# Optimization experiments

Hardware: AMD Instinct MI355X
Metric: run time of the kernel (lower is better)

Reference implementation:

```python
import jax, jax.numpy as jnp
import numpy as np

B, LP, NC, D, E = 8, 1000, 64, 128, 320  # batch, protein len, compound atoms, hid dim, esm dim


def _linear_params(key, din, dout):
    k1, k2 = jax.random.split(key)
    lim = 1.0 / np.sqrt(din)
    W = jax.random.uniform(k1, (din, dout), minval=-lim, maxval=lim, dtype=jnp.float32)
    b = jax.random.uniform(k2, (dout,), minval=-lim, maxval=lim, dtype=jnp.float32)
    return W, b


def setup_inputs() -> dict:
    key = jax.random.key(0)
    ks = jax.random.split(key, 14)
    inp = {
        "protein_embedding": jax.random.normal(ks[0], (B, LP, E), dtype=jnp.float32),
        "protein_feat_x": jax.random.normal(ks[1], (B, LP, D), dtype=jnp.float32),
        "compound_feats": jax.random.normal(ks[2], (B, NC, D), dtype=jnp.float32),
    }
    layers = [("emb", E, D), ("wq", D, D), ("wk", D, D), ("wv", D, D), ("wo", D, D),
              ("jp", D, D), ("jc", D, D),
              ("c1", D, 1024), ("c2", 1024, 1024), ("c3", 1024, 256), ("c4", 256, 1)]
    for i, (name, din, dout) in enumerate(layers):
        W, b = _linear_params(ks[3 + i], din, dout)
        inp[name + "_w"] = W
        inp[name + "_b"] = b
    return inp


def reference(protein_embedding, protein_feat_x, compound_feats,
              emb_w, emb_b, wq_w, wq_b, wk_w, wk_b, wv_w, wv_b, wo_w, wo_b,
              jp_w, jp_b, jc_w, jc_b,
              c1_w, c1_b, c2_w, c2_b, c3_w, c3_b, c4_w, c4_b):
    # protein sequence embedding -> hid dim
    pe = protein_embedding @ emb_w + emb_b                      # [B, LP, D]
    # single-head cross attention: query = seq embedding, key/value = graph feats
    Q = pe @ wq_w + wq_b
    K = protein_feat_x @ wk_w + wk_b
    V = protein_feat_x @ wv_w + wv_b
    scale = jnp.sqrt(jnp.asarray(D, pe.dtype))                  # n_heads=1 -> head_dim=D
    attn = jax.nn.softmax(jnp.einsum('bqd,bkd->bqk', Q, K) / scale, axis=-1)
    protein_feats = jnp.einsum('bqk,bkd->bqd', attn, V) @ wo_w + wo_b  # [B, LP, D]

    # sigmoid bilinear joint attention over (protein residue, compound atom) pairs
    P = jax.nn.relu(protein_feats) @ jp_w + jp_b                # [B, LP, D]
    C = jax.nn.relu(compound_feats) @ jc_w + jc_b               # [B, NC, D]
    A = jax.nn.sigmoid(jnp.einsum('bid,bkd->bik', P, C))        # [B, LP, NC]
    A = A / jnp.sum(A, axis=(1, 2), keepdims=True)

    # tanh outer product (the costly 4D bikj intermediate) then weighted reduction
    cp = jnp.tanh(protein_feats[:, :, None, :] * compound_feats[:, None, :, :])  # [B, LP, NC, D]
    cp_embedding = jnp.einsum('bikd,bik->bd', cp, A)            # [B, D]

    # classifier MLP (dropout is eval-mode identity)
    h = jax.nn.relu(cp_embedding @ c1_w + c1_b)
    h = jax.nn.relu(h @ c2_w + c2_b)
    h = jax.nn.relu(h @ c3_w + c3_b)
    return h @ c4_w + c4_b                                      # [B, 1]
```

## Files before the change

### kernel.cpp

```cpp
#include <hip/hip_runtime.h>
#include <hip/hip_bf16.h>
#include <math.h>

#define LP 1000
#define NCMP 64
#define NSPLIT 4

typedef _Float16 f16;
typedef f16   v8h __attribute__((ext_vector_type(8)));
typedef float v4f __attribute__((ext_vector_type(4)));

__device__ __forceinline__ float rcp_fast(float x) { return __builtin_amdgcn_rcpf(x); }
__device__ __forceinline__ void fsplit(float x, f16& h, f16& l) {
    h = (f16)x; l = (f16)(x - (float)h);
}

struct H4 { f16 a, b, c, d; };

__device__ __forceinline__ void gemm_core(float (*Ws)[128], float (*Xt)[36],
                                          const float* X, const float* W, const float* bias,
                                          float* Y, int K, int rowbase, bool relu_in)
{
    const int t  = threadIdx.x;
    const int r0 = (t >> 5) * 4;
    const int c0 = (t & 31) * 4;
    const int xr = t >> 3, xk = (t & 7) << 2;
    const int xrow = rowbase + xr;
    float4 xv = *(const float4*)(X + (long)xrow * K + xk);
    float4 wv[4];
    #pragma unroll
    for (int u = 0; u < 4; ++u) {
        int s = t + u * 256, r = s >> 5, cb = (s & 31) << 2;
        wv[u] = *(const float4*)(W + (long)r * 128 + cb);
    }
    float acc[4][4] = {};
    for (int k0 = 0; k0 < K; k0 += 32) {
        float4 xs = xv;
        if (relu_in) { xs.x = fmaxf(xs.x,0.f); xs.y = fmaxf(xs.y,0.f);
                       xs.z = fmaxf(xs.z,0.f); xs.w = fmaxf(xs.w,0.f); }
        Xt[xk+0][xr] = xs.x; Xt[xk+1][xr] = xs.y; Xt[xk+2][xr] = xs.z; Xt[xk+3][xr] = xs.w;
        #pragma unroll
        for (int u = 0; u < 4; ++u) {
            int s = t + u * 256, r = s >> 5, cb = (s & 31) << 2;
            *(float4*)&Ws[r][cb] = wv[u];
        }
        __syncthreads();
        if (k0 + 32 < K) {
            xv = *(const float4*)(X + (long)xrow * K + k0 + 32 + xk);
            #pragma unroll
            for (int u = 0; u < 4; ++u) {
                int s = t + u * 256, r = s >> 5, cb = (s & 31) << 2;
                wv[u] = *(const float4*)(W + (long)(k0 + 32 + r) * 128 + cb);
            }
        }
        #pragma unroll
        for (int kk = 0; kk < 32; ++kk) {
            float4 w4 = *(const float4*)&Ws[kk][c0];
            float4 x4 = *(const float4*)&Xt[kk][r0];
            acc[0][0] = fmaf(x4.x, w4.x, acc[0][0]); acc[0][1] = fmaf(x4.x, w4.y, acc[0][1]);
            acc[0][2] = fmaf(x4.x, w4.z, acc[0][2]); acc[0][3] = fmaf(x4.x, w4.w, acc[0][3]);
            acc[1][0] = fmaf(x4.y, w4.x, acc[1][0]); acc[1][1] = fmaf(x4.y, w4.y, acc[1][1]);
            acc[1][2] = fmaf(x4.y, w4.z, acc[1][2]); acc[1][3] = fmaf(x4.y, w4.w, acc[1][3]);
            acc[2][0] = fmaf(x4.z, w4.x, acc[2][0]); acc[2][1] = fmaf(x4.z, w4.y, acc[2][1]);
            acc[2][2] = fmaf(x4.z, w4.z, acc[2][2]); acc[2][3] = fmaf(x4.z, w4.w, acc[2][3]);
            acc[3][0] = fmaf(x4.w, w4.x, acc[3][0]); acc[3][1] = fmaf(x4.w, w4.y, acc[3][1]);
            acc[3][2] = fmaf(x4.w, w4.z, acc[3][2]); acc[3][3] = fmaf(x4.w, w4.w, acc[3][3]);
        }
        __syncthreads();
    }
    float4 bv = bias ? *(const float4*)(bias + c0) : make_float4(0.f,0.f,0.f,0.f);
    #pragma unroll
    for (int i = 0; i < 4; ++i) {
        int row = rowbase + r0 + i;
        float4 o;
        o.x = acc[i][0] + bv.x; o.y = acc[i][1] + bv.y;
        o.z = acc[i][2] + bv.z; o.w = acc[i][3] + bv.w;
        *(float4*)(Y + (long)row * 128 + c0) = o;
    }
}

__global__ __launch_bounds__(256) void pre0_k(const float* __restrict__ emb_w, const float* __restrict__ emb_b,
                                              const float* __restrict__ wq_w, const float* __restrict__ wq_b,
                                              const float* __restrict__ wv_w, const float* __restrict__ wv_b,
                                              const float* __restrict__ wo_w, const float* __restrict__ wo_b,
                                              float* __restrict__ Wp, float* __restrict__ bp,
                                              float* __restrict__ Wvo, float* __restrict__ bvo,
                                              float* __restrict__ zbase)
{
    __shared__ __align__(16) float Ws[32][128];
    __shared__ __align__(16) float Xt[32][36];
    const int bid = blockIdx.x;
    if (bid < 10) { gemm_core(Ws, Xt, emb_w, wq_w, nullptr, Wp, 128, bid * 32, false); return; }
    if (bid >= 11 && bid < 15) { gemm_core(Ws, Xt, wv_w, wo_w, nullptr, Wvo, 128, (bid - 11) * 32, false); return; }
    int t = threadIdx.x;
    if (bid == 10 && t >= 128) {
        for (int i = t - 128; i < 1032; i += 128) zbase[i] = 0.f;
        return;
    }
    if (t < 128) {
        const float* vb = (bid == 10) ? emb_b : wv_b;
        const float* Wm = (bid == 10) ? wq_w  : wo_w;
        const float* ab = (bid == 10) ? wq_b  : wo_b;
        float a0 = 0.f, a1 = 0.f, a2 = 0.f, a3 = 0.f;
        for (int k = 0; k < 128; k += 4) {
            a0 = fmaf(vb[k+0], Wm[(k+0)*128 + t], a0);
            a1 = fmaf(vb[k+1], Wm[(k+1)*128 + t], a1);
            a2 = fmaf(vb[k+2], Wm[(k+2)*128 + t], a2);
            a3 = fmaf(vb[k+3], Wm[(k+3)*128 + t], a3);
        }
        float* dst = (bid == 10) ? bp : bvo;
        dst[t] = (a0 + a1) + (a2 + a3) + ab[t];
    }
}

__global__ __launch_bounds__(256) void split_k(
    const float* __restrict__ PE, const float* __restrict__ PFX,
    const float* __restrict__ Wp, const float* __restrict__ wk_w,
    f16* __restrict__ PEhi, f16* __restrict__ PElo,
    f16* __restrict__ PXhi, f16* __restrict__ PXlo,
    f16* __restrict__ Vthi, f16* __restrict__ Vtlo,
    f16* __restrict__ WpThi, f16* __restrict__ WpTlo,
    f16* __restrict__ WkThi, f16* __restrict__ WkTlo)
{
    const int bid = blockIdx.x, t = threadIdx.x;
    if (bid < 250) {
        #pragma unroll
        for (int u = 0; u < 10; ++u) {
            int f = t + u * 256, r = f / 80, c = (f - r * 80) * 4;
            int grow = bid * 32 + r;
            int bb = grow / 1000, rr = grow - bb * 1000;
            float4 v = *(const float4*)(PE + (long)grow * 320 + c);
            H4 h, l;
            fsplit(v.x, h.a, l.a); fsplit(v.y, h.b, l.b);
            fsplit(v.z, h.c, l.c); fsplit(v.w, h.d, l.d);
            long o = ((long)bb * 1024 + rr) * 320 + c;
            *(H4*)(PEhi + o) = h; *(H4*)(PElo + o) = l;
        }
        return;
    }
    if (bid < 500) {
        const int rb = (bid - 250) * 32;
        #pragma unroll
        for (int u = 0; u < 4; ++u) {
            int f = t + u * 256, r = f >> 5, c = (f & 31) * 4;
            int grow = rb + r;
            int bb = grow / 1000, rr = grow - bb * 1000;
            float4 v = *(const float4*)(PFX + (long)grow * 128 + c);
            H4 h, l;
            fsplit(v.x, h.a, l.a); fsplit(v.y, h.b, l.b);
            fsplit(v.z, h.c, l.c); fsplit(v.w, h.d, l.d);
            long o = ((long)bb * 1024 + rr) * 128 + c;
            *(H4*)(PXhi + o) = h; *(H4*)(PXlo + o) = l;
        }
        const int d = t >> 1, half = t & 1;
        #pragma unroll 4
        for (int i = 0; i < 16; ++i) {
            int row = rb + half * 16 + i;
            int bb = row / 1000, rr = row - bb * 1000;
            float v = PFX[(long)row * 128 + d];
            f16 h, l; fsplit(v, h, l);
            long o = ((long)bb * 128 + d) * 1024 + rr;
            Vthi[o] = h; Vtlo[o] = l;
        }
        return;
    }
    #pragma unroll
    for (int u = 0; u < 8; ++u) {
        int idx = (bid - 500) * 2048 + u * 256 + t;
        if (idx < 40960) {
            int k = idx >> 7, n = idx & 127;
            f16 h, l; fsplit(Wp[idx], h, l);
            WpThi[(long)n * 320 + k] = h; WpTlo[(long)n * 320 + k] = l;
        } else {
            int j = idx - 40960;
            int k = j >> 7, n = j & 127;
            f16 h, l; fsplit(wk_w[j], h, l);
            WkThi[(long)n * 128 + k] = h; WkTlo[(long)n * 128 + k] = l;
        }
    }
}

__global__ __launch_bounds__(256) void qkv2_k(
    const f16* __restrict__ PEhi, const f16* __restrict__ PElo,
    const f16* __restrict__ PXhi, const f16* __restrict__ PXlo,
    const f16* __restrict__ WpThi, const f16* __restrict__ WpTlo,
    const f16* __restrict__ WkThi, const f16* __restrict__ WkTlo,
    const float* __restrict__ bp, const float* __restrict__ wk_b,
    const float* __restrict__ CF, const float* __restrict__ jc_w, const float* __restrict__ jc_b,
    f16* __restrict__ Qhi, f16* __restrict__ Qlo,
    f16* __restrict__ Khi, f16* __restrict__ Klo,
    float* __restrict__ Cj)
{
    __shared__ __align__(16) float Ws[32][128];
    __shared__ __align__(16) float Xt[32][36];
    const int bid = blockIdx.x;
    if (bid >= 256) { gemm_core(Ws, Xt, CF, jc_w, jc_b, Cj, 128, (bid - 256) * 32, true); return; }
    const bool isQ = bid < 128;
    const int b = (bid & 127) >> 4, tile = bid & 15;
    const int KD  = isQ ? 320 : 128;
    const int NCH = isQ ? 10 : 4;
    const f16* Ahi = isQ ? PEhi : PXhi;
    const f16* Alo = isQ ? PElo : PXlo;
    const f16* Bhi = isQ ? WpThi : WkThi;
    const f16* Blo = isQ ? WpTlo : WkTlo;
    const float* bias = isQ ? bp : wk_b;
    f16* Yhi = isQ ? Qhi : Khi;
    f16* Ylo = isQ ? Qlo : Klo;

    const int t = threadIdx.x;
    const int wv = t >> 6, lane = t & 63, quad = lane >> 4, l4 = lane & 15;
    int arow = tile * 64 + wv * 16 + l4; if (arow >= LP) arow = LP - 1;
    const f16* ah_p = Ahi + ((long)b * 1024 + arow) * KD;
    const f16* al_p = Alo + ((long)b * 1024 + arow) * KD;

    v4f acc[8];
    #pragma unroll
    for (int dt = 0; dt < 8; ++dt) acc[dt] = (v4f){0.f, 0.f, 0.f, 0.f};

    for (int kt = 0; kt < NCH; ++kt) {
        const int ko = kt * 32 + quad * 8;
        v8h ah = *(const v8h*)(ah_p + ko);
        v8h al = *(const v8h*)(al_p + ko);
        #pragma unroll
        for (int dt = 0; dt < 8; ++dt) {
            const long bo = (long)(dt * 16 + l4) * KD + ko;
            v8h bh = *(const v8h*)(Bhi + bo);
            v8h bl = *(const v8h*)(Blo + bo);
            acc[dt] = __builtin_amdgcn_mfma_f32_16x16x32_f16(ah, bh, acc[dt], 0, 0, 0);
            acc[dt] = __builtin_amdgcn_mfma_f32_16x16x32_f16(ah, bl, acc[dt], 0, 0, 0);
            acc[dt] = __builtin_amdgcn_mfma_f32_16x16x32_f16(al, bh, acc[dt], 0, 0, 0);
        }
    }
    #pragma unroll
    for (int dt = 0; dt < 8; ++dt) {
        const int col = dt * 16 + l4;
        const float bv = bias[col];
        #pragma unroll
        for (int r = 0; r < 4; ++r) {
            int row = tile * 64 + wv * 16 + quad * 4 + r;
            long o = ((long)b * 1024 + row) * 128 + col;
            f16 h, l; fsplit(acc[dt][r] + bv, h, l);
            Yhi[o] = h; Ylo[o] = l;
        }
    }
}

__global__ __launch_bounds__(256) void flash7_k(const f16* __restrict__ Qhi, const f16* __restrict__ Qlo,
                                                const f16* __restrict__ Khi, const f16* __restrict__ Klo,
                                                const f16* __restrict__ Vthi, const f16* __restrict__ Vtlo,
                                                float* __restrict__ Opart,
                                                float* __restrict__ mpart, float* __restrict__ lpart)
{
    __shared__ __align__(16) f16 KVhi[9216];
    __shared__ __align__(16) f16 KVlo[9216];
    __shared__ __align__(16) f16 Pshi[4][16 * 72];
    __shared__ __align__(16) f16 Pslo[4][16 * 72];
    const int t    = threadIdx.x;
    const int wv   = t >> 6;
    const int lane = t & 63;
    const int quad = lane >> 4;
    const int l4   = lane & 15;
    const int qt = blockIdx.x, sp = blockIdx.y, b = blockIdx.z;
    const int q0 = qt * 64;
    const float SCALE = 0.08838834764831845f;
    const float L2E   = 1.4426950408889634f;

    int qrow = q0 + wv * 16 + l4; if (qrow >= LP) qrow = LP - 1;
    const long qbase = ((long)b * 1024 + qrow) * 128;
    v8h qh[4], ql[4];
    #pragma unroll
    for (int kt4 = 0; kt4 < 4; ++kt4) {
        qh[kt4] = *(const v8h*)(Qhi + qbase + kt4 * 32 + quad * 8);
        ql[kt4] = *(const v8h*)(Qlo + qbase + kt4 * 32 + quad * 8);
    }
    float m_i[4] = { -3.0e38f, -3.0e38f, -3.0e38f, -3.0e38f };
    float l_i[4] = { 0.f, 0.f, 0.f, 0.f };
    v4f  O[8];
    #pragma unroll
    for (int dt = 0; dt < 8; ++dt) O[dt] = (v4f){0.f, 0.f, 0.f, 0.f};

    for (int kt = sp * 4; kt < sp * 4 + 4; ++kt) {
        const int key0 = kt * 64;
        __syncthreads();
        #pragma unroll
        for (int u = 0; u < 4; ++u) {
            int ch = t + u * 256;
            int r = ch >> 4, co = (ch & 15) * 8;
            long ga = ((long)b * 1024 + key0 + r) * 128 + co;
            *(v8h*)(KVhi + r * 136 + co) = *(const v8h*)(Khi + ga);
            *(v8h*)(KVlo + r * 136 + co) = *(const v8h*)(Klo + ga);
        }
        __syncthreads();
        v8h vh[4], vl[4];
        #pragma unroll
        for (int u = 0; u < 4; ++u) {
            int ch = t + u * 256;
            int d = ch >> 3, co = (ch & 7) * 8;
            long ga = ((long)b * 128 + d) * 1024 + key0 + co;
            vh[u] = *(const v8h*)(Vthi + ga);
            vl[u] = *(const v8h*)(Vtlo + ga);
        }
        v4f S[4];
        #pragma unroll
        for (int nt = 0; nt < 4; ++nt) S[nt] = (v4f){0.f, 0.f, 0.f, 0.f};
        #pragma unroll
        for (int nt = 0; nt < 4; ++nt) {
            const int rb = (nt * 16 + l4) * 136;
            #pragma unroll
            for (int kt4 = 0; kt4 < 4; ++kt4) {
                v8h bh = *(const v8h*)(KVhi + rb + kt4 * 32 + quad * 8);
                v8h bl = *(const v8h*)(KVlo + rb + kt4 * 32 + quad * 8);
                S[nt] = __builtin_amdgcn_mfma_f32_16x16x32_f16(qh[kt4], bh, S[nt], 0, 0, 0);
                S[nt] = __builtin_amdgcn_mfma_f32_16x16x32_f16(qh[kt4], bl, S[nt], 0, 0, 0);
                S[nt] = __builtin_amdgcn_mfma_f32_16x16x32_f16(ql[kt4], bh, S[nt], 0, 0, 0);
            }
        }
        #pragma unroll
        for (int nt = 0; nt < 4; ++nt) {
            bool valid = (key0 + nt * 16 + l4) < LP;
            #pragma unroll
            for (int r = 0; r < 4; ++r)
                S[nt][r] = valid ? S[nt][r] * SCALE : -3.0e38f;
        }
        float alpha[4];
        #pragma unroll
        for (int r = 0; r < 4; ++r) {
            float tm = fmaxf(fmaxf(S[0][r], S[1][r]), fmaxf(S[2][r], S[3][r]));
            tm = fmaxf(tm, __shfl_xor(tm, 1));
            tm = fmaxf(tm, __shfl_xor(tm, 2));
            tm = fmaxf(tm, __shfl_xor(tm, 4));
            tm = fmaxf(tm, __shfl_xor(tm, 8));
            float mnew = fmaxf(m_i[r], tm);
            alpha[r] = exp2f((m_i[r] - mnew) * L2E);
            float ps = 0.f;
            #pragma unroll
            for (int nt = 0; nt < 4; ++nt) {
                float p = exp2f((S[nt][r] - mnew) * L2E);
                S[nt][r] = p;
                ps += p;
            }
            ps += __shfl_xor(ps, 1);
            ps += __shfl_xor(ps, 2);
            ps += __shfl_xor(ps, 4);
            ps += __shfl_xor(ps, 8);
            l_i[r] = l_i[r] * alpha[r] + ps;
            m_i[r] = mnew;
        }
        #pragma unroll
        for (int dt = 0; dt < 8; ++dt) {
            O[dt][0] *= alpha[0]; O[dt][1] *= alpha[1];
            O[dt][2] *= alpha[2]; O[dt][3] *= alpha[3];
        }
        __syncthreads();
        #pragma unroll
        for (int u = 0; u < 4; ++u) {
            int ch = t + u * 256;
            int d = ch >> 3, co = (ch & 7) * 8;
            *(v8h*)(KVhi + d * 72 + co) = vh[u];
            *(v8h*)(KVlo + d * 72 + co) = vl[u];
        }
        #pragma unroll
        for (int nt = 0; nt < 4; ++nt) {
            int col = nt * 16 + l4;
            #pragma unroll
            for (int r = 0; r < 4; ++r) {
                f16 ph, pl; fsplit(S[nt][r], ph, pl);
                Pshi[wv][(quad * 4 + r) * 72 + col] = ph;
                Pslo[wv][(quad * 4 + r) * 72 + col] = pl;
            }
        }
        __syncthreads();
        #pragma unroll
        for (int kc = 0; kc < 2; ++kc) {
            v8h pah = *(const v8h*)(Pshi[wv] + l4 * 72 + kc * 32 + quad * 8);
            v8h pal = *(const v8h*)(Pslo[wv] + l4 * 72 + kc * 32 + quad * 8);
            #pragma unroll
            for (int dt = 0; dt < 8; ++dt) {
                v8h vfh = *(const v8h*)(KVhi + (dt * 16 + l4) * 72 + kc * 32 + quad * 8);
                v8h vfl = *(const v8h*)(KVlo + (dt * 16 + l4) * 72 + kc * 32 + quad * 8);
                O[dt] = __builtin_amdgcn_mfma_f32_16x16x32_f16(pah, vfh, O[dt], 0, 0, 0);
                O[dt] = __builtin_amdgcn_mfma_f32_16x16x32_f16(pah, vfl, O[dt], 0, 0, 0);
                O[dt] = __builtin_amdgcn_mfma_f32_16x16x32_f16(pal, vfh, O[dt], 0, 0, 0);
            }
        }
    }
    #pragma unroll
    for (int r = 0; r < 4; ++r) {
        int row = q0 + wv * 16 + quad * 4 + r;
        if (row < LP) {
            long base = (long)sp * 1024000 + ((long)b * LP + row) * 128;
            #pragma unroll
            for (int dt = 0; dt < 8; ++dt)
                Opart[base + dt * 16 + l4] = O[dt][r];
            if (l4 == 0) {
                mpart[(long)sp * 8000 + b * LP + row] = m_i[r];
                lpart[(long)sp * 8000 + b * LP + row] = l_i[r];
            }
        }
    }
}

__global__ __launch_bounds__(256) void mt1a_k(
    const float* __restrict__ Opart, const float* __restrict__ mp, const float* __restrict__ lp,
    const float* __restrict__ Wvo, const float* __restrict__ bvo, float* __restrict__ PF)
{
    __shared__ __align__(16) float Ws[128][128];
    __shared__ __align__(16) float Xs[16][132];
    const int t  = threadIdx.x;
    const int p0 = blockIdx.x * 16;
    const int b  = blockIdx.y;
    const float L2E = 1.4426950408889634f;

    #pragma unroll
    for (int u = 0; u < 16; ++u) {
        int s = t + u * 256, r = s >> 5, cb = (s & 31) << 2;
        *(float4*)&Ws[r][cb] = *(const float4*)(Wvo + (long)r * 128 + cb);
    }
    {
        const int pr = t >> 4, pc = (t & 15) << 3;
        int grow = p0 + pr; if (grow > LP - 1) grow = LP - 1;
        const long g = (long)b * LP + grow;
        float mm = -3.0e38f;
        #pragma unroll
        for (int s = 0; s < NSPLIT; ++s) mm = fmaxf(mm, mp[g + (long)s * 8000]);
        float wgt[NSPLIT]; float ls = 0.f;
        #pragma unroll
        for (int s = 0; s < NSPLIT; ++s) {
            wgt[s] = exp2f((mp[g + (long)s * 8000] - mm) * L2E);
            ls += wgt[s] * lp[g + (long)s * 8000];
        }
        const float linv = 1.0f / ls;
        float4 a0 = make_float4(0.f,0.f,0.f,0.f), a1 = make_float4(0.f,0.f,0.f,0.f);
        #pragma unroll
        for (int s = 0; s < NSPLIT; ++s) {
            const float* src = Opart + (long)s * 1024000 + g * 128 + pc;
            float4 p = *(const float4*)src;
            float4 q = *(const float4*)(src + 4);
            a0.x = fmaf(wgt[s], p.x, a0.x); a0.y = fmaf(wgt[s], p.y, a0.y);
            a0.z = fmaf(wgt[s], p.z, a0.z); a0.w = fmaf(wgt[s], p.w, a0.w);
            a1.x = fmaf(wgt[s], q.x, a1.x); a1.y = fmaf(wgt[s], q.y, a1.y);
            a1.z = fmaf(wgt[s], q.z, a1.z); a1.w = fmaf(wgt[s], q.w, a1.w);
        }
        *(float4*)&Xs[pr][pc]     = make_float4(a0.x*linv, a0.y*linv, a0.z*linv, a0.w*linv);
        *(float4*)&Xs[pr][pc + 4] = make_float4(a1.x*linv, a1.y*linv, a1.z*linv, a1.w*linv);
    }
    __syncthreads();
    const int r0 = (t >> 5) * 2;
    const int c0 = (t & 31) * 4;
    float acc[2][4] = {};
    #pragma unroll 8
    for (int kk4 = 0; kk4 < 128; kk4 += 4) {
        float4 xa = *(const float4*)&Xs[r0 + 0][kk4];
        float4 xb = *(const float4*)&Xs[r0 + 1][kk4];
        #pragma unroll
        for (int j = 0; j < 4; ++j) {
            float4 w4 = *(const float4*)&Ws[kk4 + j][c0];
            float x0 = (j==0)?xa.x:(j==1)?xa.y:(j==2)?xa.z:xa.w;
            float x1 = (j==0)?xb.x:(j==1)?xb.y:(j==2)?xb.z:xb.w;
            acc[0][0]=fmaf(x0,w4.x,acc[0][0]); acc[0][1]=fmaf(x0,w4.y,acc[0][1]);
            acc[0][2]=fmaf(x0,w4.z,acc[0][2]); acc[0][3]=fmaf(x0,w4.w,acc[0][3]);
            acc[1][0]=fmaf(x1,w4.x,acc[1][0]); acc[1][1]=fmaf(x1,w4.y,acc[1][1]);
            acc[1][2]=fmaf(x1,w4.z,acc[1][2]); acc[1][3]=fmaf(x1,w4.w,acc[1][3]);
        }
    }
    float4 bv = *(const float4*)(bvo + c0);
    #pragma unroll
    for (int i = 0; i < 2; ++i) {
        int orow = p0 + r0 + i;
        if (orow < LP)
            *(float4*)(PF + ((long)b * LP + orow) * 128 + c0) =
                make_float4(acc[i][0]+bv.x, acc[i][1]+bv.y, acc[i][2]+bv.z, acc[i][3]+bv.w);
    }
}

__global__ __launch_bounds__(256) void mt1b_k(
    const float* __restrict__ PF, const float* __restrict__ jp_w, const float* __restrict__ jp_b,
    float* __restrict__ PJ)
{
    __shared__ __align__(16) float Ws[128][128];
    __shared__ __align__(16) float Xs[16][132];
    const int t  = threadIdx.x;
    const int p0 = blockIdx.x * 16;
    const int b  = blockIdx.y;

    #pragma unroll
    for (int u = 0; u < 16; ++u) {
        int s = t + u * 256, r = s >> 5, cb = (s & 31) << 2;
        *(float4*)&Ws[r][cb] = *(const float4*)(jp_w + (long)r * 128 + cb);
    }
    {
        const int pr = t >> 4, pc = (t & 15) << 3;
        int grow = p0 + pr; if (grow > LP - 1) grow = LP - 1;
        const float* src = PF + ((long)b * LP + grow) * 128 + pc;
        float4 p = *(const float4*)src;
        float4 q = *(const float4*)(src + 4);
        *(float4*)&Xs[pr][pc] =
            make_float4(fmaxf(p.x,0.f), fmaxf(p.y,0.f), fmaxf(p.z,0.f), fmaxf(p.w,0.f));
        *(float4*)&Xs[pr][pc + 4] =
            make_float4(fmaxf(q.x,0.f), fmaxf(q.y,0.f), fmaxf(q.z,0.f), fmaxf(q.w,0.f));
    }
    __syncthreads();
    const int r0 = (t >> 5) * 2;
    const int c0 = (t & 31) * 4;
    float acc[2][4] = {};
    #pragma unroll 8
    for (int kk4 = 0; kk4 < 128; kk4 += 4) {
        float4 xa = *(const float4*)&Xs[r0 + 0][kk4];
        float4 xb = *(const float4*)&Xs[r0 + 1][kk4];
        #pragma unroll
        for (int j = 0; j < 4; ++j) {
            float4 w4 = *(const float4*)&Ws[kk4 + j][c0];
            float x0 = (j==0)?xa.x:(j==1)?xa.y:(j==2)?xa.z:xa.w;
            float x1 = (j==0)?xb.x:(j==1)?xb.y:(j==2)?xb.z:xb.w;
            acc[0][0]=fmaf(x0,w4.x,acc[0][0]); acc[0][1]=fmaf(x0,w4.y,acc[0][1]);
            acc[0][2]=fmaf(x0,w4.z,acc[0][2]); acc[0][3]=fmaf(x0,w4.w,acc[0][3]);
            acc[1][0]=fmaf(x1,w4.x,acc[1][0]); acc[1][1]=fmaf(x1,w4.y,acc[1][1]);
            acc[1][2]=fmaf(x1,w4.z,acc[1][2]); acc[1][3]=fmaf(x1,w4.w,acc[1][3]);
        }
    }
    float4 bv = *(const float4*)(jp_b + c0);
    #pragma unroll
    for (int i = 0; i < 2; ++i) {
        int orow = p0 + r0 + i;
        if (orow < LP)
            *(float4*)(PJ + ((long)b * LP + orow) * 128 + c0) =
                make_float4(acc[i][0]+bv.x, acc[i][1]+bv.y, acc[i][2]+bv.z, acc[i][3]+bv.w);
    }
}

template<int IIN>
__device__ __forceinline__ float tanh_chunk(const float (*Cs)[132], const float (*AshT)[20],
                                            const float* areg, int d, int kh)
{
    float accD = 0.f;
    for (int kk = 0; kk < 16; ++kk) {
        const int k = (kh << 4) + kk;
        const float cv = Cs[k][d];
        #pragma unroll
        for (int iq = 0; iq < IIN; iq += 4) {
            float4 a4 = *(const float4*)&AshT[k][iq];
            float e0 = exp2f(areg[iq+0] * cv);
            float e1 = exp2f(areg[iq+1] * cv);
            float e2 = exp2f(areg[iq+2] * cv);
            float e3 = exp2f(areg[iq+3] * cv);
            accD = fmaf(1.f - 2.f * rcp_fast(e0 + 1.f), a4.x, accD);
            accD = fmaf(1.f - 2.f * rcp_fast(e1 + 1.f), a4.y, accD);
            accD = fmaf(1.f - 2.f * rcp_fast(e2 + 1.f), a4.z, accD);
            accD = fmaf(1.f - 2.f * rcp_fast(e3 + 1.f), a4.w, accD);
        }
    }
    return accD;
}

__global__ __launch_bounds__(256) void mt2_k(
    const float* __restrict__ PF, const float* __restrict__ PJ,
    const float* __restrict__ Cj, const float* __restrict__ CF,
    float* __restrict__ Asum, float* __restrict__ cpe)
{
    __shared__ __align__(16) float Pjs[16][132];
    __shared__ __align__(16) float Pfs[16][132];
    __shared__ __align__(16) float Cs[32][132];
    __shared__ __align__(16) float AshT[32][20];
    __shared__ float red[256];
    const int t  = threadIdx.x;
    const int p0 = blockIdx.x * 16;
    const int kc = blockIdx.y;
    const int b  = blockIdx.z;
    const float L2E = 1.4426950408889634f;

    {
        int pr = t >> 4, pc = (t & 15) << 3;
        int gr = p0 + pr; if (gr > LP - 1) gr = LP - 1;
        long gb = ((long)b * LP + gr) * 128 + pc;
        *(float4*)&Pjs[pr][pc]     = *(const float4*)(PJ + gb);
        *(float4*)&Pjs[pr][pc + 4] = *(const float4*)(PJ + gb + 4);
        *(float4*)&Pfs[pr][pc]     = *(const float4*)(PF + gb);
        *(float4*)&Pfs[pr][pc + 4] = *(const float4*)(PF + gb + 4);
    }
    float4 cfv[4];
    #pragma unroll
    for (int u = 0; u < 4; ++u) {
        int s = t + u * 256, r = s >> 5, cb = (s & 31) << 2;
        *(float4*)&Cs[r][cb] = *(const float4*)(Cj + ((long)b * NCMP + kc * 32 + r) * 128 + cb);
        cfv[u] = *(const float4*)(CF + ((long)b * NCMP + kc * 32 + r) * 128 + cb);
    }
    __syncthreads();
    const int tr = t >> 4, tc = t & 15;
    float sacc[2] = {0.f, 0.f};
    #pragma unroll 4
    for (int d4 = 0; d4 < 32; ++d4) {
        float4 p4 = *(const float4*)&Pjs[tr][d4 << 2];
        #pragma unroll
        for (int j = 0; j < 2; ++j) {
            float4 cv = *(const float4*)&Cs[tc + (j << 4)][d4 << 2];
            sacc[j] += p4.x*cv.x + p4.y*cv.y + p4.z*cv.z + p4.w*cv.w;
        }
    }
    float lsum = 0.f;
    const int gi = p0 + tr;
    #pragma unroll
    for (int j = 0; j < 2; ++j) {
        float sg = rcp_fast(1.f + exp2f(-sacc[j] * L2E));
        if (gi < LP) { AshT[tc + (j << 4)][tr] = sg; lsum += sg; }
    }
    #pragma unroll
    for (int off = 1; off < 64; off <<= 1) lsum += __shfl_xor(lsum, off);
    if ((t & 63) == 0) red[t >> 6] = lsum;
    __syncthreads();
    if (t == 0) atomicAdd(Asum + b, (red[0] + red[1]) + (red[2] + red[3]));
    #pragma unroll
    for (int u = 0; u < 4; ++u) {
        int s = t + u * 256, r = s >> 5, cb = (s & 31) << 2;
        *(float4*)&Cs[r][cb] = cfv[u];
    }
    __syncthreads();
    const float TWO_L2E = 2.8853900817779268f;
    const int d = t & 127, kh = t >> 7;
    float areg[16];
    #pragma unroll
    for (int ii = 0; ii < 16; ++ii) areg[ii] = Pfs[ii][d] * TWO_L2E;
    float accD = (p0 + 16 <= LP) ? tanh_chunk<16>(Cs, AshT, areg, d, kh)
                                 : tanh_chunk<8>(Cs, AshT, areg, d, kh);
    red[t] = accD;
    __syncthreads();
    if (t < 128) atomicAdd(cpe + (long)b * 128 + t, red[t] + red[t + 128]);
}

__global__ __launch_bounds__(256) void c12_k(const float* __restrict__ cpe, const float* __restrict__ Asum,
                                             const float* __restrict__ c1_w, const float* __restrict__ c1_b,
                                             const float* __restrict__ c2_w, float* __restrict__ part)
{
    __shared__ float sc[8][128];
    __shared__ float ins[8][8];
    const int t = threadIdx.x, ks = blockIdx.x, k0 = ks * 8;
    #pragma unroll
    for (int u = 0; u < 4; ++u) {
        int idx = t + u * 256;
        sc[idx >> 7][idx & 127] = cpe[idx] * rcp_fast(Asum[idx >> 7]);
    }
    __syncthreads();
    if (t < 64) {
        int b = t >> 3, kk = t & 7;
        int n1 = k0 + kk;
        float a0 = 0.f, a1 = 0.f, a2 = 0.f, a3 = 0.f;
        #pragma unroll 8
        for (int j = 0; j < 128; j += 4) {
            a0 = fmaf(sc[b][j+0], c1_w[(long)(j+0)*1024 + n1], a0);
            a1 = fmaf(sc[b][j+1], c1_w[(long)(j+1)*1024 + n1], a1);
            a2 = fmaf(sc[b][j+2], c1_w[(long)(j+2)*1024 + n1], a2);
            a3 = fmaf(sc[b][j+3], c1_w[(long)(j+3)*1024 + n1], a3);
        }
        ins[b][kk] = fmaxf((a0 + a1) + (a2 + a3) + c1_b[n1], 0.f);
    }
    __syncthreads();
    const int n = (t & 63) * 4 + (t >> 6) * 256;
    float4 acc[8] = {};
    #pragma unroll
    for (int kk = 0; kk < 8; ++kk) {
        float4 w4 = *(const float4*)(c2_w + (long)(k0 + kk) * 1024 + n);
        #pragma unroll
        for (int b = 0; b < 8; ++b) {
            float s = ins[b][kk];
            acc[b].x = fmaf(s, w4.x, acc[b].x); acc[b].y = fmaf(s, w4.y, acc[b].y);
            acc[b].z = fmaf(s, w4.z, acc[b].z); acc[b].w = fmaf(s, w4.w, acc[b].w);
        }
    }
    #pragma unroll
    for (int b = 0; b < 8; ++b)
        *(float4*)(part + ((long)(ks * 8 + b)) * 1024 + n) = acc[b];
}

__global__ __launch_bounds__(256) void c3m_k(const float* __restrict__ part2, const float* __restrict__ c2_b,
                                             const float* __restrict__ c3_w, const float* __restrict__ c3_b,
                                             const float* __restrict__ c4_w, const float* __restrict__ c4_b,
                                             float* __restrict__ out)
{
    __shared__ float Hs[1024];
    __shared__ float red[256];
    const int t = threadIdx.x, b = blockIdx.x;
    float4 acc4 = make_float4(0.f,0.f,0.f,0.f);
    #pragma unroll 4
    for (int ks = 0; ks < 128; ++ks) {
        float4 p = *(const float4*)(part2 + ((long)(ks * 8 + b)) * 1024 + t * 4);
        acc4.x += p.x; acc4.y += p.y; acc4.z += p.z; acc4.w += p.w;
    }
    {
        float4 bb = *(const float4*)(c2_b + t * 4);
        Hs[t*4+0] = fmaxf(acc4.x + bb.x, 0.f);
        Hs[t*4+1] = fmaxf(acc4.y + bb.y, 0.f);
        Hs[t*4+2] = fmaxf(acc4.z + bb.z, 0.f);
        Hs[t*4+3] = fmaxf(acc4.w + bb.w, 0.f);
    }
    __syncthreads();
    float a0 = 0.f, a1 = 0.f, a2 = 0.f, a3 = 0.f;
    #pragma unroll 8
    for (int k = 0; k < 1024; k += 4) {
        a0 = fmaf(Hs[k+0], c3_w[(long)(k+0)*256 + t], a0);
        a1 = fmaf(Hs[k+1], c3_w[(long)(k+1)*256 + t], a1);
        a2 = fmaf(Hs[k+2], c3_w[(long)(k+2)*256 + t], a2);
        a3 = fmaf(Hs[k+3], c3_w[(long)(k+3)*256 + t], a3);
    }
    float h3v = fmaxf((a0 + a1) + (a2 + a3) + c3_b[t], 0.f);
    red[t] = h3v * c4_w[t];
    __syncthreads();
    for (int off = 128; off > 0; off >>= 1) {
        if (t < off) red[t] += red[t + off];
        __syncthreads();
    }
    if (t == 0) out[b] = red[0] + c4_b[0];
}

extern "C" void kernel_launch(void* const* d_in, const int* in_sizes, int n_in,
                              void* d_out, int out_size, void* d_ws, size_t ws_size,
                              hipStream_t stream)
{
    const float* PE   = (const float*)d_in[0];
    const float* PFX  = (const float*)d_in[1];
    const float* CF   = (const float*)d_in[2];
    const float* emb_w = (const float*)d_in[3];  const float* emb_b = (const float*)d_in[4];
    const float* wq_w  = (const float*)d_in[5];  const float* wq_b  = (const float*)d_in[6];
    const float* wk_w  = (const float*)d_in[7];  const float* wk_b  = (const float*)d_in[8];
    const float* wv_w  = (const float*)d_in[9];  const float* wv_b  = (const float*)d_in[10];
    const float* wo_w  = (const float*)d_in[11]; const float* wo_b  = (const float*)d_in[12];
    const float* jp_w  = (const float*)d_in[13]; const float* jp_b  = (const float*)d_in[14];
    const float* jc_w  = (const float*)d_in[15]; const float* jc_b  = (const float*)d_in[16];
    const float* c1_w  = (const float*)d_in[17]; const float* c1_b  = (const float*)d_in[18];
    const float* c2_w  = (const float*)d_in[19]; const float* c2_b  = (const float*)d_in[20];
    const float* c3_w  = (const float*)d_in[21]; const float* c3_b  = (const float*)d_in[22];
    const float* c4_w  = (const float*)d_in[23]; const float* c4_b  = (const float*)d_in[24];

    float* ws     = (float*)d_ws;
    f16*  Qhi   = (f16*)ws;
    f16*  Qlo   = (f16*)(ws + 524288);
    f16*  Khi   = (f16*)(ws + 1048576);
    f16*  Klo   = (f16*)(ws + 1572864);
    f16*  Vthi  = (f16*)(ws + 2097152);
    f16*  Vtlo  = (f16*)(ws + 2621440);
    float* bufC   = ws + 3145728;
    float* Opart  = bufC + 65536;
    float* mpart  = Opart + 4096000;
    float* lpart  = mpart + 32000;
    float* Asum   = lpart + 32000;
    float* cpe    = Asum + 8;
    float* bprime = cpe + 1024;
    float* bufWp  = bprime + 128;
    float* bufWvo = bufWp + 40960;
    float* bufbvo = bufWvo + 16384;
    float* part2  = ws;
    float* PFbuf  = ws + 1048576;
    float* PJbuf  = ws + 2097152;
    f16* PEhi  = (f16*)(ws + 7430144);
    f16* PElo  = (f16*)(ws + 8740864);
    f16* PXhi  = (f16*)(ws + 10051584);
    f16* PXlo  = (f16*)(ws + 10575872);
    f16* WpThi = (f16*)(ws + 11100160);
    f16* WpTlo = (f16*)(ws + 11120640);
    f16* WkThi = (f16*)(ws + 11141120);
    f16* WkTlo = (f16*)(ws + 11149312);

    pre0_k<<<16, 256, 0, stream>>>(emb_w, emb_b, wq_w, wq_b, wv_w, wv_b, wo_w, wo_b,
                                   bufWp, bprime, bufWvo, bufbvo, Asum);
    split_k<<<528, 256, 0, stream>>>(PE, PFX, bufWp, wk_w,
                                     PEhi, PElo, PXhi, PXlo, Vthi, Vtlo,
                                     WpThi, WpTlo, WkThi, WkTlo);
    qkv2_k<<<272, 256, 0, stream>>>(PEhi, PElo, PXhi, PXlo,
                                    WpThi, WpTlo, WkThi, WkTlo,
                                    bprime, wk_b, CF, jc_w, jc_b,
                                    Qhi, Qlo, Khi, Klo, bufC);
    flash7_k<<<dim3(16, NSPLIT, 8), 256, 0, stream>>>(Qhi, Qlo, Khi, Klo, Vthi, Vtlo,
                                                      Opart, mpart, lpart);
    mt1a_k<<<dim3(63, 8), 256, 0, stream>>>(Opart, mpart, lpart, bufWvo, bufbvo, PFbuf);
    mt1b_k<<<dim3(63, 8), 256, 0, stream>>>(PFbuf, jp_w, jp_b, PJbuf);
    mt2_k<<<dim3(63, 2, 8), 256, 0, stream>>>(PFbuf, PJbuf, bufC, CF, Asum, cpe);
    c12_k<<<128, 256, 0, stream>>>(cpe, Asum, c1_w, c1_b, c2_w, part2);
    c3m_k<<<8, 256, 0, stream>>>(part2, c2_b, c3_w, c3_b, c4_w, c4_b, (float*)d_out);
}
```

Before: 282.3 us.

## Fuse fp16 hi/lo split into QKV GEMM and merge mt1a/mt1b kernels

The QKV MFMA kernel now reads the fp32 protein embedding and graph features directly and splits them into fp16 hi/lo pairs in registers. This removes the separate pass that wrote PEhi/PElo/PXhi/PXlo to global memory and read them back. The attention-output projection and the jp projection kernels are also merged into one kernel, which passes the relu'd PF tile through shared memory instead of reloading it from global memory. In exchange the GEMM does redundant conversion work per tile, and one launch is dropped.

```diff
diff --git a/kernel.cpp b/kernel.cpp
--- a/kernel.cpp
+++ b/kernel.cpp
@@ -13,6 +13,15 @@
 __device__ __forceinline__ float rcp_fast(float x) { return __builtin_amdgcn_rcpf(x); }
 __device__ __forceinline__ void fsplit(float x, f16& h, f16& l) {
     h = (f16)x; l = (f16)(x - (float)h);
+}
+__device__ __forceinline__ void fs8(const float4& f0, const float4& f1, v8h& h, v8h& l) {
+    const float x[8] = {f0.x, f0.y, f0.z, f0.w, f1.x, f1.y, f1.z, f1.w};
+    #pragma unroll
+    for (int i = 0; i < 8; ++i) {
+        f16 hh = (f16)x[i];
+        h[i] = hh;
+        l[i] = (f16)(x[i] - (float)hh);
+    }
 }
 
 struct H4 { f16 a, b, c, d; };
@@ -113,45 +122,15 @@
     }
 }
 
-__global__ __launch_bounds__(256) void split_k(
-    const float* __restrict__ PE, const float* __restrict__ PFX,
-    const float* __restrict__ Wp, const float* __restrict__ wk_w,
-    f16* __restrict__ PEhi, f16* __restrict__ PElo,
-    f16* __restrict__ PXhi, f16* __restrict__ PXlo,
+__global__ __launch_bounds__(256) void prep_k(
+    const float* __restrict__ PFX, const float* __restrict__ Wp, const float* __restrict__ wk_w,
     f16* __restrict__ Vthi, f16* __restrict__ Vtlo,
     f16* __restrict__ WpThi, f16* __restrict__ WpTlo,
     f16* __restrict__ WkThi, f16* __restrict__ WkTlo)
 {
     const int bid = blockIdx.x, t = threadIdx.x;
     if (bid < 250) {
-        #pragma unroll
-        for (int u = 0; u < 10; ++u) {
-            int f = t + u * 256, r = f / 80, c = (f - r * 80) * 4;
-            int grow = bid * 32 + r;
-            int bb = grow / 1000, rr = grow - bb * 1000;
-            float4 v = *(const float4*)(PE + (long)grow * 320 + c);
-            H4 h, l;
-            fsplit(v.x, h.a, l.a); fsplit(v.y, h.b, l.b);
-            fsplit(v.z, h.c, l.c); fsplit(v.w, h.d, l.d);
-            long o = ((long)bb * 1024 + rr) * 320 + c;
-            *(H4*)(PEhi + o) = h; *(H4*)(PElo + o) = l;
-        }
-        return;
-    }
-    if (bid < 500) {
-        const int rb = (bid - 250) * 32;
-        #pragma unroll
-        for (int u = 0; u < 4; ++u) {
-            int f = t + u * 256, r = f >> 5, c = (f & 31) * 4;
-            int grow = rb + r;
-            int bb = grow / 1000, rr = grow - bb * 1000;
-            float4 v = *(const float4*)(PFX + (long)grow * 128 + c);
-            H4 h, l;
-            fsplit(v.x, h.a, l.a); fsplit(v.y, h.b, l.b);
-            fsplit(v.z, h.c, l.c); fsplit(v.w, h.d, l.d);
-            long o = ((long)bb * 1024 + rr) * 128 + c;
-            *(H4*)(PXhi + o) = h; *(H4*)(PXlo + o) = l;
-        }
+        const int rb = bid * 32;
         const int d = t >> 1, half = t & 1;
         #pragma unroll 4
         for (int i = 0; i < 16; ++i) {
@@ -166,12 +145,12 @@
     }
     #pragma unroll
     for (int u = 0; u < 8; ++u) {
-        int idx = (bid - 500) * 2048 + u * 256 + t;
+        int idx = (bid - 250) * 2048 + u * 256 + t;
         if (idx < 40960) {
             int k = idx >> 7, n = idx & 127;
             f16 h, l; fsplit(Wp[idx], h, l);
             WpThi[(long)n * 320 + k] = h; WpTlo[(long)n * 320 + k] = l;
-        } else {
+        } else if (idx < 57344) {
             int j = idx - 40960;
             int k = j >> 7, n = j & 127;
             f16 h, l; fsplit(wk_w[j], h, l);
@@ -180,9 +159,8 @@
     }
 }
 
-__global__ __launch_bounds__(256) void qkv2_k(
-    const f16* __restrict__ PEhi, const f16* __restrict__ PElo,
-    const f16* __restrict__ PXhi, const f16* __restrict__ PXlo,
+__global__ __launch_bounds__(256) void qkv3_k(
+    const float* __restrict__ PE, const float* __restrict__ PFX,
     const f16* __restrict__ WpThi, const f16* __restrict__ WpTlo,
     const f16* __restrict__ WkThi, const f16* __restrict__ WkTlo,
     const float* __restrict__ bp, const float* __restrict__ wk_b,
@@ -199,8 +177,7 @@
     const int b = (bid & 127) >> 4, tile = bid & 15;
     const int KD  = isQ ? 320 : 128;
     const int NCH = isQ ? 10 : 4;
-    const f16* Ahi = isQ ? PEhi : PXhi;
-    const f16* Alo = isQ ? PElo : PXlo;
+    const float* A = isQ ? PE : PFX;
     const f16* Bhi = isQ ? WpThi : WkThi;
     const f16* Blo = isQ ? WpTlo : WkTlo;
     const float* bias = isQ ? bp : wk_b;
@@ -210,8 +187,7 @@
     const int t = threadIdx.x;
     const int wv = t >> 6, lane = t & 63, quad = lane >> 4, l4 = lane & 15;
     int arow = tile * 64 + wv * 16 + l4; if (arow >= LP) arow = LP - 1;
-    const f16* ah_p = Ahi + ((long)b * 1024 + arow) * KD;
-    const f16* al_p = Alo + ((long)b * 1024 + arow) * KD;
+    const float* a_p = A + ((long)b * LP + arow) * KD;
 
     v4f acc[8];
     #pragma unroll
@@ -219,8 +195,10 @@
 
     for (int kt = 0; kt < NCH; ++kt) {
         const int ko = kt * 32 + quad * 8;
-        v8h ah = *(const v8h*)(ah_p + ko);
-        v8h al = *(const v8h*)(al_p + ko);
+        float4 f0 = *(const float4*)(a_p + ko);
+        float4 f1 = *(const float4*)(a_p + ko + 4);
+        v8h ah, al;
+        fs8(f0, f1, ah, al);
         #pragma unroll
         for (int dt = 0; dt < 8; ++dt) {
             const long bo = (long)(dt * 16 + l4) * KD + ko;
@@ -400,9 +378,11 @@
     }
 }
 
-__global__ __launch_bounds__(256) void mt1a_k(
+__global__ __launch_bounds__(256) void mt1ab_k(
     const float* __restrict__ Opart, const float* __restrict__ mp, const float* __restrict__ lp,
-    const float* __restrict__ Wvo, const float* __restrict__ bvo, float* __restrict__ PF)
+    const float* __restrict__ Wvo, const float* __restrict__ bvo,
+    const float* __restrict__ jp_w, const float* __restrict__ jp_b,
+    float* __restrict__ PF, float* __restrict__ PJ)
 {
     __shared__ __align__(16) float Ws[128][128];
     __shared__ __align__(16) float Xs[16][132];
@@ -410,6 +390,8 @@
     const int p0 = blockIdx.x * 16;
     const int b  = blockIdx.y;
     const float L2E = 1.4426950408889634f;
+    const int r0 = (t >> 5) * 2;
+    const int c0 = (t & 31) * 4;
 
     #pragma unroll
     for (int u = 0; u < 16; ++u) {
@@ -445,8 +427,6 @@
         *(float4*)&Xs[pr][pc + 4] = make_float4(a1.x*linv, a1.y*linv, a1.z*linv, a1.w*linv);
     }
     __syncthreads();
-    const int r0 = (t >> 5) * 2;
-    const int c0 = (t & 31) * 4;
     float acc[2][4] = {};
     #pragma unroll 8
     for (int kk4 = 0; kk4 < 128; kk4 += 4) {
@@ -463,46 +443,26 @@
             acc[1][2]=fmaf(x1,w4.z,acc[1][2]); acc[1][3]=fmaf(x1,w4.w,acc[1][3]);
         }
     }
-    float4 bv = *(const float4*)(bvo + c0);
-    #pragma unroll
-    for (int i = 0; i < 2; ++i) {
-        int orow = p0 + r0 + i;
-        if (orow < LP)
-            *(float4*)(PF + ((long)b * LP + orow) * 128 + c0) =
-                make_float4(acc[i][0]+bv.x, acc[i][1]+bv.y, acc[i][2]+bv.z, acc[i][3]+bv.w);
-    }
-}
-
-__global__ __launch_bounds__(256) void mt1b_k(
-    const float* __restrict__ PF, const float* __restrict__ jp_w, const float* __restrict__ jp_b,
-    float* __restrict__ PJ)
-{
-    __shared__ __align__(16) float Ws[128][128];
-    __shared__ __align__(16) float Xs[16][132];
-    const int t  = threadIdx.x;
-    const int p0 = blockIdx.x * 16;
-    const int b  = blockIdx.y;
-
+    __syncthreads();
     #pragma unroll
     for (int u = 0; u < 16; ++u) {
         int s = t + u * 256, r = s >> 5, cb = (s & 31) << 2;
         *(float4*)&Ws[r][cb] = *(const float4*)(jp_w + (long)r * 128 + cb);
     }
     {
-        const int pr = t >> 4, pc = (t & 15) << 3;
-        int grow = p0 + pr; if (grow > LP - 1) grow = LP - 1;
-        const float* src = PF + ((long)b * LP + grow) * 128 + pc;
-        float4 p = *(const float4*)src;
-        float4 q = *(const float4*)(src + 4);
-        *(float4*)&Xs[pr][pc] =
-            make_float4(fmaxf(p.x,0.f), fmaxf(p.y,0.f), fmaxf(p.z,0.f), fmaxf(p.w,0.f));
-        *(float4*)&Xs[pr][pc + 4] =
-            make_float4(fmaxf(q.x,0.f), fmaxf(q.y,0.f), fmaxf(q.z,0.f), fmaxf(q.w,0.f));
-    }
-    __syncthreads();
-    const int r0 = (t >> 5) * 2;
-    const int c0 = (t & 31) * 4;
-    float acc[2][4] = {};
+        float4 bv = *(const float4*)(bvo + c0);
+        #pragma unroll
+        for (int i = 0; i < 2; ++i) {
+            float4 o = make_float4(acc[i][0]+bv.x, acc[i][1]+bv.y, acc[i][2]+bv.z, acc[i][3]+bv.w);
+            int orow = p0 + r0 + i;
+            if (orow < LP)
+                *(float4*)(PF + ((long)b * LP + orow) * 128 + c0) = o;
+            *(float4*)&Xs[r0 + i][c0] =
+                make_float4(fmaxf(o.x,0.f), fmaxf(o.y,0.f), fmaxf(o.z,0.f), fmaxf(o.w,0.f));
+        }
+    }
+    __syncthreads();
+    float ac2[2][4] = {};
     #pragma unroll 8
     for (int kk4 = 0; kk4 < 128; kk4 += 4) {
         float4 xa = *(const float4*)&Xs[r0 + 0][kk4];
@@ -512,19 +472,19 @@
             float4 w4 = *(const float4*)&Ws[kk4 + j][c0];
             float x0 = (j==0)?xa.x:(j==1)?xa.y:(j==2)?xa.z:xa.w;
             float x1 = (j==0)?xb.x:(j==1)?xb.y:(j==2)?xb.z:xb.w;
-            acc[0][0]=fmaf(x0,w4.x,acc[0][0]); acc[0][1]=fmaf(x0,w4.y,acc[0][1]);
-            acc[0][2]=fmaf(x0,w4.z,acc[0][2]); acc[0][3]=fmaf(x0,w4.w,acc[0][3]);
-            acc[1][0]=fmaf(x1,w4.x,acc[1][0]); acc[1][1]=fmaf(x1,w4.y,acc[1][1]);
-            acc[1][2]=fmaf(x1,w4.z,acc[1][2]); acc[1][3]=fmaf(x1,w4.w,acc[1][3]);
-        }
-    }
-    float4 bv = *(const float4*)(jp_b + c0);
+            ac2[0][0]=fmaf(x0,w4.x,ac2[0][0]); ac2[0][1]=fmaf(x0,w4.y,ac2[0][1]);
+            ac2[0][2]=fmaf(x0,w4.z,ac2[0][2]); ac2[0][3]=fmaf(x0,w4.w,ac2[0][3]);
+            ac2[1][0]=fmaf(x1,w4.x,ac2[1][0]); ac2[1][1]=fmaf(x1,w4.y,ac2[1][1]);
+            ac2[1][2]=fmaf(x1,w4.z,ac2[1][2]); ac2[1][3]=fmaf(x1,w4.w,ac2[1][3]);
+        }
+    }
+    float4 b2 = *(const float4*)(jp_b + c0);
     #pragma unroll
     for (int i = 0; i < 2; ++i) {
         int orow = p0 + r0 + i;
         if (orow < LP)
             *(float4*)(PJ + ((long)b * LP + orow) * 128 + c0) =
-                make_float4(acc[i][0]+bv.x, acc[i][1]+bv.y, acc[i][2]+bv.z, acc[i][3]+bv.w);
+                make_float4(ac2[i][0]+b2.x, ac2[i][1]+b2.y, ac2[i][2]+b2.z, ac2[i][3]+b2.w);
     }
 }
 
@@ -749,28 +709,22 @@
     float* part2  = ws;
     float* PFbuf  = ws + 1048576;
     float* PJbuf  = ws + 2097152;
-    f16* PEhi  = (f16*)(ws + 7430144);
-    f16* PElo  = (f16*)(ws + 8740864);
-    f16* PXhi  = (f16*)(ws + 10051584);
-    f16* PXlo  = (f16*)(ws + 10575872);
-    f16* WpThi = (f16*)(ws + 11100160);
-    f16* WpTlo = (f16*)(ws + 11120640);
-    f16* WkThi = (f16*)(ws + 11141120);
-    f16* WkTlo = (f16*)(ws + 11149312);
+    f16* WpThi = (f16*)(ws + 7430144);
+    f16* WpTlo = (f16*)(ws + 7450624);
+    f16* WkThi = (f16*)(ws + 7471104);
+    f16* WkTlo = (f16*)(ws + 7479296);
 
     pre0_k<<<16, 256, 0, stream>>>(emb_w, emb_b, wq_w, wq_b, wv_w, wv_b, wo_w, wo_b,
                                    bufWp, bprime, bufWvo, bufbvo, Asum);
-    split_k<<<528, 256, 0, stream>>>(PE, PFX, bufWp, wk_w,
-                                     PEhi, PElo, PXhi, PXlo, Vthi, Vtlo,
-                                     WpThi, WpTlo, WkThi, WkTlo);
-    qkv2_k<<<272, 256, 0, stream>>>(PEhi, PElo, PXhi, PXlo,
-                                    WpThi, WpTlo, WkThi, WkTlo,
+    prep_k<<<278, 256, 0, stream>>>(PFX, bufWp, wk_w, Vthi, Vtlo,
+                                    WpThi, WpTlo, WkThi, WkTlo);
+    qkv3_k<<<272, 256, 0, stream>>>(PE, PFX, WpThi, WpTlo, WkThi, WkTlo,
                                     bprime, wk_b, CF, jc_w, jc_b,
                                     Qhi, Qlo, Khi, Klo, bufC);
     flash7_k<<<dim3(16, NSPLIT, 8), 256, 0, stream>>>(Qhi, Qlo, Khi, Klo, Vthi, Vtlo,
                                                       Opart, mpart, lpart);
-    mt1a_k<<<dim3(63, 8), 256, 0, stream>>>(Opart, mpart, lpart, bufWvo, bufbvo, PFbuf);
-    mt1b_k<<<dim3(63, 8), 256, 0, stream>>>(PFbuf, jp_w, jp_b, PJbuf);
+    mt1ab_k<<<dim3(63, 8), 256, 0, stream>>>(Opart, mpart, lpart, bufWvo, bufbvo,
+                                             jp_w, jp_b, PFbuf, PJbuf);
     mt2_k<<<dim3(63, 2, 8), 256, 0, stream>>>(PFbuf, PJbuf, bufC, CF, Asum, cpe);
     c12_k<<<128, 256, 0, stream>>>(cpe, Asum, c1_w, c1_b, c2_w, part2);
     c3m_k<<<8, 256, 0, stream>>>(part2, c2_b, c3_w, c3_b, c4_w, c4_b, (float*)d_out);
```

After: 283.1 us. No clear change (+0.3%).
